# Kernel tuning notes

Hardware: AMD Instinct MI355X
Metric: run time of the kernel (lower is better)

## Reference

```python
import jax, jax.numpy as jnp
import numpy as np

D_MAIN = 512
D_BLOCK = 1024
N_NUM = 50
N_CAT = 20
N_FREQ = 16
D_EMB = 16
D_IN = N_NUM * D_EMB + N_CAT  # 820
EPS = 1e-5


def _ln(x, g, b):
    m = jnp.mean(x, -1, keepdims=True)
    v = jnp.mean((x - m) ** 2, -1, keepdims=True)
    return (x - m) * jax.lax.rsqrt(v + EPS) * g + b


def _encode(x_num, x_cat, freq, plr_w, plr_b, lin_w, lin_b,
            enc_w1, enc_b1, enc_w2, enc_b2, mix_g, mix_b, K_w, K_b):
    # PLR embeddings (lite): (B, F) -> (B, F, 2*n_freq) -> (B, F, d_emb) -> flatten
    p = 2.0 * jnp.pi * freq[None] * x_num[..., None]          # (B, F, n_freq)
    e = jnp.concatenate([jnp.cos(p), jnp.sin(p)], -1)          # (B, F, 2*n_freq)
    e = jax.nn.relu(e @ plr_w + plr_b)                         # (B, F, d_emb)
    x = jnp.concatenate([e.reshape(x_num.shape[0], -1), x_cat], 1)  # (B, d_in)
    x = x @ lin_w + lin_b                                      # (B, d_main)
    # encoder block 0 (no prenorm since i == 0); dropouts are 0 in eval
    x = x + (jax.nn.relu(x @ enc_w1 + enc_b1) @ enc_w2 + enc_b2)
    k = _ln(x, mix_g, mix_b) @ K_w + K_b                       # mixer normalization then K
    return x, k


def setup_inputs() -> dict:
    key = jax.random.key(0)
    ks = jax.random.split(key, 40)
    s = 0.02
    inp = {
        "x_num": jax.random.normal(ks[0], (512, N_NUM), jnp.float32),
        "x_cat": jax.random.uniform(ks[1], (512, N_CAT), jnp.float32),
        "candidate_x_num": jax.random.normal(ks[2], (50000, N_NUM), jnp.float32),
        "candidate_x_cat": jax.random.uniform(ks[3], (50000, N_CAT), jnp.float32),
        "candidate_y": jax.random.normal(ks[4], (50000,), jnp.float32),
        "context_size": 96,
        # PLR embedding params
        "freq": jax.random.normal(ks[5], (N_NUM, N_FREQ), jnp.float32) * 0.1,
        "plr_w": jax.random.normal(ks[6], (2 * N_FREQ, D_EMB), jnp.float32) * s,
        "plr_b": jnp.zeros((D_EMB,), jnp.float32),
        # input linear
        "lin_w": jax.random.normal(ks[7], (D_IN, D_MAIN), jnp.float32) * s,
        "lin_b": jnp.zeros((D_MAIN,), jnp.float32),
        # encoder block 0
        "enc_w1": jax.random.normal(ks[8], (D_MAIN, D_BLOCK), jnp.float32) * s,
        "enc_b1": jnp.zeros((D_BLOCK,), jnp.float32),
        "enc_w2": jax.random.normal(ks[9], (D_BLOCK, D_MAIN), jnp.float32) * s,
        "enc_b2": jnp.zeros((D_MAIN,), jnp.float32),
        # mixer normalization
        "mix_g": jnp.ones((D_MAIN,), jnp.float32),
        "mix_b": jnp.zeros((D_MAIN,), jnp.float32),
        # K projection
        "K_w": jax.random.normal(ks[10], (D_MAIN, D_MAIN), jnp.float32) * s,
        "K_b": jnp.zeros((D_MAIN,), jnp.float32),
        # label encoder Linear(1, d_main), uniform(-1/sqrt(2), 1/sqrt(2))
        "label_w": jax.random.uniform(ks[11], (D_MAIN,), jnp.float32, -0.7071, 0.7071),
        "label_b": jax.random.uniform(ks[12], (D_MAIN,), jnp.float32, -0.7071, 0.7071),
        # T transform
        "T_w1": jax.random.normal(ks[13], (D_MAIN, D_BLOCK), jnp.float32) * s,
        "T_b1": jnp.zeros((D_BLOCK,), jnp.float32),
        "T_w2": jax.random.normal(ks[14], (D_BLOCK, D_MAIN), jnp.float32) * s,
        # predictor block (prenorm)
        "pred_g": jnp.ones((D_MAIN,), jnp.float32),
        "pred_b": jnp.zeros((D_MAIN,), jnp.float32),
        "pred_w1": jax.random.normal(ks[15], (D_MAIN, D_BLOCK), jnp.float32) * s,
        "pred_b1": jnp.zeros((D_BLOCK,), jnp.float32),
        "pred_w2": jax.random.normal(ks[16], (D_BLOCK, D_MAIN), jnp.float32) * s,
        "pred_b2": jnp.zeros((D_MAIN,), jnp.float32),
        # head: LayerNorm -> ReLU -> Linear(d_main, 1)
        "head_g": jnp.ones((D_MAIN,), jnp.float32),
        "head_b": jnp.zeros((D_MAIN,), jnp.float32),
        "head_w": jax.random.normal(ks[17], (D_MAIN, 1), jnp.float32) * s,
        "head_bias": jnp.zeros((1,), jnp.float32),
    }
    return inp


def reference(x_num, x_cat, candidate_x_num, candidate_x_cat, candidate_y, context_size,
              freq, plr_w, plr_b, lin_w, lin_b, enc_w1, enc_b1, enc_w2, enc_b2,
              mix_g, mix_b, K_w, K_b, label_w, label_b, T_w1, T_b1, T_w2,
              pred_g, pred_b, pred_w1, pred_b1, pred_w2, pred_b2,
              head_g, head_b, head_w, head_bias):
    enc = lambda xn, xc: _encode(xn, xc, freq, plr_w, plr_b, lin_w, lin_b,
                                 enc_w1, enc_b1, enc_w2, enc_b2, mix_g, mix_b, K_w, K_b)
    # candidate keys cached under no_grad in the original
    cand_k = jax.lax.stop_gradient(enc(candidate_x_num, candidate_x_cat)[1])  # (N, D)
    x, k = enc(x_num, x_cat)                                                  # (B, D)
    # exact L2 kNN (= FAISS GpuIndexFlatL2), under no_grad
    kq = jax.lax.stop_gradient(k)
    d2 = (jnp.sum(kq * kq, -1, keepdims=True)
          - 2.0 * kq @ cand_k.T
          + jnp.sum(cand_k * cand_k, -1))                                     # (B, N)
    _, ctx_idx = jax.lax.top_k(-d2, context_size)                             # (B, C)
    ctx_k = cand_k[ctx_idx]                                                   # (B, C, D)
    # differentiable similarities (negative squared L2)
    sim = (-jnp.sum(k * k, -1, keepdims=True)
           + 2.0 * jnp.einsum('bd,bcd->bc', k, ctx_k)
           - jnp.sum(ctx_k * ctx_k, -1))                                      # (B, C)
    probs = jax.nn.softmax(sim, -1)                                           # (B, C)
    ctx_y = candidate_y[ctx_idx]                                              # (B, C)
    y_emb = ctx_y[..., None] * label_w + label_b                              # (B, C, D)
    diff = k[:, None, :] - ctx_k                                              # (B, C, D)
    values = y_emb + jax.nn.relu(diff @ T_w1 + T_b1) @ T_w2                   # (B, C, D)
    x = x + jnp.einsum('bc,bcd->bd', probs, values)
    # predictor block (prenorm)
    h = _ln(x, pred_g, pred_b)
    x = x + (jax.nn.relu(h @ pred_w1 + pred_b1) @ pred_w2 + pred_b2)
    # head
    return jax.nn.relu(_ln(x, head_g, head_b)) @ head_w + head_bias           # (B, 1)
```

## Files before the change

kernel.cpp:

```cpp
#include <hip/hip_runtime.h>

#define NCAND 50000
#define NB    512
#define DIN   820
#define KP_IN 832
#define DM    512
#define DBK   1024
#define NFEAT 50
#define NCAT  20
#define NFREQ 16
#define DEMB  16
#define CTX   96
#define NCMAX 9216
#define TOTMAX (NCMAX + CTX)

typedef __attribute__((ext_vector_type(8))) short short8;
typedef __attribute__((ext_vector_type(4))) float f32x4;

static __device__ __forceinline__ unsigned short f2bf(float f) {
    union { float f; unsigned int i; } u; u.f = f;
    unsigned int r = u.i + 0x7FFFu + ((u.i >> 16) & 1u);
    return (unsigned short)(r >> 16);
}
static __device__ __forceinline__ float bf2f(unsigned short s) {
    union { unsigned int i; float f; } u; u.i = ((unsigned int)s) << 16;
    return u.f;
}
static __device__ __forceinline__ unsigned int f2key(float f) {
    union { float f; unsigned int i; } u; u.f = f;
    return (u.i & 0x80000000u) ? ~u.i : (u.i | 0x80000000u);
}
static __device__ __forceinline__ float key2f(unsigned int k) {
    union { unsigned int i; float f; } u;
    u.i = (k & 0x80000000u) ? (k ^ 0x80000000u) : ~k;
    return u.f;
}

#define GLDS16(g, l) __builtin_amdgcn_global_load_lds( \
    (const __attribute__((address_space(1))) void*)(g), \
    (__attribute__((address_space(3))) void*)(l), 16, 0, 0)

#define BG_RELU  1
#define BG_SCORE 2

static __device__ __forceinline__ int swizzle_blk(int L, int nbx, int nby, int bigx,
                                                  int* bx, int* by)
{
    int nsm = bigx ? nby : nbx;
    int xcd = L & 7, slot = L >> 3;
    int big = xcd + 8 * (slot / nsm);
    int sml = slot % nsm;
    *bx = bigx ? big : sml;
    *by = bigx ? sml : big;
    return (*bx < nbx) && (*by < nby);
}

__global__ __launch_bounds__(256) void wprep_kernel(
    const float* __restrict__ W, int K, int N, int Kp,
    unsigned short* __restrict__ Wh, unsigned short* __restrict__ Wl)
{
    int idx = blockIdx.x * 256 + threadIdx.x;
    if (idx >= N * Kp) return;
    int n = idx / Kp, k = idx % Kp;
    float v = (k < K) ? W[(size_t)k * N + n] : 0.f;
    unsigned short h = f2bf(v);
    Wh[idx] = h;
    if (Wl) Wl[idx] = f2bf(v - bf2f(h));
}

__global__ __launch_bounds__(256) void plr_bf16_kernel(
    const float* __restrict__ xn_, const float* __restrict__ xc_, int nrows,
    const float* __restrict__ freq, const float* __restrict__ plr_w,
    const float* __restrict__ plr_b,
    unsigned short* __restrict__ oh, unsigned short* __restrict__ ol)
{
    __shared__ float sW[32 * 16];
    __shared__ float sB[16];
    __shared__ float sF[NFEAT * NFREQ];
    int tid = threadIdx.x;
    for (int i = tid; i < 512; i += 256) sW[i] = plr_w[i];
    if (tid < 16) sB[tid] = plr_b[tid];
    for (int i = tid; i < NFEAT * NFREQ; i += 256) sF[i] = freq[i];
    __syncthreads();
    int wave = tid >> 6, lane = tid & 63;
    int row = blockIdx.x * 4 + wave;
    if (row >= nrows) return;
    const float* xn = xn_ + (size_t)row * NFEAT;
    const float* xc = xc_ + (size_t)row * NCAT;
    unsigned short* ph = oh + (size_t)row * KP_IN;
    unsigned short* pl = ol + (size_t)row * KP_IN;
    if (lane < NFEAT) {
        float x = xn[lane];
        float cs[NFREQ], sn[NFREQ];
        #pragma unroll
        for (int j = 0; j < NFREQ; j++) {
            float p = 6.28318530717958647692f * sF[lane * NFREQ + j] * x;
            sn[j] = __sinf(p);
            cs[j] = __cosf(p);
        }
        #pragma unroll
        for (int d = 0; d < DEMB; d++) {
            float acc = sB[d];
            #pragma unroll
            for (int j = 0; j < NFREQ; j++)
                acc = fmaf(cs[j], sW[j * DEMB + d], fmaf(sn[j], sW[(NFREQ + j) * DEMB + d], acc));
            float v = fmaxf(acc, 0.f);
            unsigned short h = f2bf(v);
            ph[lane * DEMB + d] = h;
            pl[lane * DEMB + d] = f2bf(v - bf2f(h));
        }
    }
    if (lane < NCAT) {
        float v = xc[lane];
        unsigned short h = f2bf(v);
        ph[800 + lane] = h;
        pl[800 + lane] = f2bf(v - bf2f(h));
    }
    if (lane >= NCAT && lane < 32) {
        ph[800 + lane] = 0;
        pl[800 + lane] = 0;
    }
}

__global__ __launch_bounds__(512) void bgemm_kernel(
    const unsigned short* __restrict__ A, const unsigned short* __restrict__ Bt,
    int M, int N, int Kp, int nbx, int nby, int bigx,
    float* __restrict__ Cf, unsigned short* __restrict__ Cb,
    const float* __restrict__ bias, int flags)
{
    __shared__ unsigned short SH[2][2][128 * 32];
    int bxi, byi;
    if (!swizzle_blk(blockIdx.x, nbx, nby, bigx, &bxi, &byi)) return;
    int tid = threadIdx.x;
    int w = tid >> 6, lane = tid & 63;
    int m0 = byi * 128, n0 = bxi * 128;
    int wr = (w >> 1) * 32, wc = (w & 1) * 64;

    f32x4 acc[2][4];
    #pragma unroll
    for (int i = 0; i < 2; i++)
        #pragma unroll
        for (int j = 0; j < 4; j++) acc[i][j] = (f32x4){0.f, 0.f, 0.f, 0.f};

    int arr = w & 1;
    int qrt = (w >> 1) * 32;
    int scol = (((lane & 3) - ((lane >> 3) & 3)) & 3) * 8;
    const unsigned short* gsrc = arr ? Bt : A;
    int glim = arr ? (N - 1) : (M - 1);
    int gb   = arr ? n0 : m0;
    const unsigned short* gp0 = gsrc + (size_t)min(gb + qrt + (lane >> 2),      glim) * Kp + scol;
    const unsigned short* gp1 = gsrc + (size_t)min(gb + qrt + 16 + (lane >> 2), glim) * Kp + scol;
    int lo0 = qrt * 32, lo1 = (qrt + 16) * 32;

    int fr = lane & 15, q = lane >> 4;
    int pcs = ((q + (fr >> 1)) & 3) * 8;
    int niter = Kp >> 5;

    GLDS16(gp0, &SH[0][arr][lo0]);
    GLDS16(gp1, &SH[0][arr][lo1]);

    for (int it = 0; it < niter; it++) {
        __syncthreads();
        int bsel = it & 1;
        if (it + 1 < niter) {
            int k1 = (it + 1) << 5;
            GLDS16(gp0 + k1, &SH[bsel ^ 1][arr][lo0]);
            GLDS16(gp1 + k1, &SH[bsel ^ 1][arr][lo1]);
        }
        const unsigned short* As = SH[bsel][0];
        const unsigned short* Bs = SH[bsel][1];
        short8 a[2], b[4];
        #pragma unroll
        for (int i = 0; i < 2; i++)
            a[i] = *(const short8*)&As[(wr + i * 16 + fr) * 32 + pcs];
        #pragma unroll
        for (int j = 0; j < 4; j++)
            b[j] = *(const short8*)&Bs[(wc + j * 16 + fr) * 32 + pcs];
        #pragma unroll
        for (int i = 0; i < 2; i++)
            #pragma unroll
            for (int j = 0; j < 4; j++)
                acc[i][j] = __builtin_amdgcn_mfma_f32_16x16x32_bf16(a[i], b[j], acc[i][j], 0, 0, 0);
    }

    int col = lane & 15, rq = (lane >> 4) * 4;
    #pragma unroll
    for (int i = 0; i < 2; i++)
        #pragma unroll
        for (int j = 0; j < 4; j++) {
            int n_g = n0 + wc + j * 16 + col;
            #pragma unroll
            for (int r = 0; r < 4; r++) {
                int m_g = m0 + wr + i * 16 + rq + r;
                if (m_g < M && n_g < N) {
                    float v = acc[i][j][r];
                    if (bias) v += bias[n_g];
                    if (flags & BG_RELU) v = fmaxf(v, 0.f);
                    if (Cf) Cf[(size_t)m_g * N + n_g] = v;
                    if (Cb) Cb[(size_t)m_g * N + n_g] = f2bf(v);
                }
            }
        }
}

__global__ __launch_bounds__(512) void bgemm3_kernel(
    const unsigned short* __restrict__ Ah, const unsigned short* __restrict__ Al,
    const unsigned short* __restrict__ Bh, const unsigned short* __restrict__ Bl,
    int M, int N, int Kp, int nbx, int nby, int bigx,
    float* __restrict__ Cf, unsigned short* __restrict__ Cbh, unsigned short* __restrict__ Cbl,
    const float* __restrict__ bias, const float* __restrict__ resf,
    const float* __restrict__ cnorm, int flags)
{
    __shared__ unsigned short SH[2][4][128 * 32];
    int bxi, byi;
    if (!swizzle_blk(blockIdx.x, nbx, nby, bigx, &bxi, &byi)) return;
    int tid = threadIdx.x;
    int w = tid >> 6, lane = tid & 63;
    int m0 = byi * 128, n0 = bxi * 128;
    int wr = (w >> 1) * 32, wc = (w & 1) * 64;

    f32x4 acc[2][4];
    #pragma unroll
    for (int i = 0; i < 2; i++)
        #pragma unroll
        for (int j = 0; j < 4; j++) acc[i][j] = (f32x4){0.f, 0.f, 0.f, 0.f};

    int arr = w & 3;
    int half = (w >> 2) * 64;
    int scol = (((lane & 3) - ((lane >> 3) & 3)) & 3) * 8;
    const unsigned short* gsrc = (arr == 0) ? Ah : (arr == 1) ? Al : (arr == 2) ? Bh : Bl;
    int glim = (arr < 2) ? (M - 1) : (N - 1);
    int gb   = (arr < 2) ? m0 : n0;
    const unsigned short* gp[4];
    int lofs[4];
    #pragma unroll
    for (int t = 0; t < 4; t++) {
        int r = half + t * 16;
        gp[t] = gsrc + (size_t)min(gb + r + (lane >> 2), glim) * Kp + scol;
        lofs[t] = r * 32;
    }

    int fr = lane & 15, q = lane >> 4;
    int pcs = ((q + (fr >> 1)) & 3) * 8;
    int niter = Kp >> 5;

    #pragma unroll
    for (int t = 0; t < 4; t++) GLDS16(gp[t], &SH[0][arr][lofs[t]]);

    for (int it = 0; it < niter; it++) {
        __syncthreads();
        int bsel = it & 1;
        if (it + 1 < niter) {
            int k1 = (it + 1) << 5;
            #pragma unroll
            for (int t = 0; t < 4; t++) GLDS16(gp[t] + k1, &SH[bsel ^ 1][arr][lofs[t]]);
        }
        const unsigned short* Ash = SH[bsel][0];
        const unsigned short* Asl = SH[bsel][1];
        const unsigned short* Bsh = SH[bsel][2];
        const unsigned short* Bsl = SH[bsel][3];
        short8 a[2], b[4];
        #pragma unroll
        for (int i = 0; i < 2; i++)
            a[i] = *(const short8*)&Ash[(wr + i * 16 + fr) * 32 + pcs];
        #pragma unroll
        for (int j = 0; j < 4; j++)
            b[j] = *(const short8*)&Bsh[(wc + j * 16 + fr) * 32 + pcs];
        #pragma unroll
        for (int i = 0; i < 2; i++)
            #pragma unroll
            for (int j = 0; j < 4; j++)
                acc[i][j] = __builtin_amdgcn_mfma_f32_16x16x32_bf16(a[i], b[j], acc[i][j], 0, 0, 0);
        short8 al2[2];
        #pragma unroll
        for (int i = 0; i < 2; i++)
            al2[i] = *(const short8*)&Asl[(wr + i * 16 + fr) * 32 + pcs];
        #pragma unroll
        for (int i = 0; i < 2; i++)
            #pragma unroll
            for (int j = 0; j < 4; j++)
                acc[i][j] = __builtin_amdgcn_mfma_f32_16x16x32_bf16(al2[i], b[j], acc[i][j], 0, 0, 0);
        short8 bl2[4];
        #pragma unroll
        for (int j = 0; j < 4; j++)
            bl2[j] = *(const short8*)&Bsl[(wc + j * 16 + fr) * 32 + pcs];
        #pragma unroll
        for (int i = 0; i < 2; i++)
            #pragma unroll
            for (int j = 0; j < 4; j++)
                acc[i][j] = __builtin_amdgcn_mfma_f32_16x16x32_bf16(a[i], bl2[j], acc[i][j], 0, 0, 0);
    }

    int col = lane & 15, rq = (lane >> 4) * 4;
    #pragma unroll
    for (int i = 0; i < 2; i++)
        #pragma unroll
        for (int j = 0; j < 4; j++) {
            int n_g = n0 + wc + j * 16 + col;
            #pragma unroll
            for (int r = 0; r < 4; r++) {
                int m_g = m0 + wr + i * 16 + rq + r;
                if (m_g < M && n_g < N) {
                    float v = acc[i][j][r];
                    if (bias) v += bias[n_g];
                    if (resf) v += resf[(size_t)m_g * N + n_g];
                    if (flags & BG_RELU) v = fmaxf(v, 0.f);
                    if (flags & BG_SCORE) v = 2.f * v - cnorm[n_g];
                    if (Cf) Cf[(size_t)m_g * N + n_g] = v;
                    if (Cbh) {
                        unsigned short h = f2bf(v);
                        Cbh[(size_t)m_g * N + n_g] = h;
                        if (Cbl) Cbl[(size_t)m_g * N + n_g] = f2bf(v - bf2f(h));
                    }
                }
            }
        }
}

__global__ __launch_bounds__(256) void bgemm3s_kernel(
    const unsigned short* __restrict__ Ah, const unsigned short* __restrict__ Al,
    const unsigned short* __restrict__ Bh, const unsigned short* __restrict__ Bl,
    int M, int N, int Kp,
    float* __restrict__ Cf, unsigned short* __restrict__ Cbh, unsigned short* __restrict__ Cbl,
    const float* __restrict__ bias, const float* __restrict__ resf, int flags)
{
    __shared__ unsigned short Ash[64 * 32];
    __shared__ unsigned short Asl[64 * 32];
    __shared__ unsigned short Bsh[64 * 32];
    __shared__ unsigned short Bsl[64 * 32];
    int tid = threadIdx.x;
    int w = tid >> 6, lane = tid & 63;
    int m0 = blockIdx.y * 64, n0 = blockIdx.x * 64;
    int wr = (w >> 1) * 32, wc = (w & 1) * 32;
    int three = (Al != nullptr);

    f32x4 acc[2][2];
    #pragma unroll
    for (int i = 0; i < 2; i++)
        #pragma unroll
        for (int j = 0; j < 2; j++) acc[i][j] = (f32x4){0.f, 0.f, 0.f, 0.f};

    int srow = w * 16 + (lane >> 2);
    int scol = (((lane & 3) - ((lane >> 3) & 3)) & 3) * 8;
    size_t ra = (size_t)min(m0 + srow, M - 1) * Kp + scol;
    size_t rb = (size_t)min(n0 + srow, N - 1) * Kp + scol;
    unsigned short* lah = &Ash[(w * 16) * 32];
    unsigned short* lal = &Asl[(w * 16) * 32];
    unsigned short* lbh = &Bsh[(w * 16) * 32];
    unsigned short* lbl = &Bsl[(w * 16) * 32];

    int fr = lane & 15, q = lane >> 4;
    int pcs = ((q + (fr >> 1)) & 3) * 8;

    for (int k0 = 0; k0 < Kp; k0 += 32) {
        __syncthreads();
        GLDS16(Ah + ra + k0, lah);
        GLDS16(Bh + rb + k0, lbh);
        if (three) {
            GLDS16(Al + ra + k0, lal);
            GLDS16(Bl + rb + k0, lbl);
        }
        __syncthreads();
        short8 a[2], b[2];
        #pragma unroll
        for (int i = 0; i < 2; i++)
            a[i] = *(const short8*)&Ash[(wr + i * 16 + fr) * 32 + pcs];
        #pragma unroll
        for (int j = 0; j < 2; j++)
            b[j] = *(const short8*)&Bsh[(wc + j * 16 + fr) * 32 + pcs];
        #pragma unroll
        for (int i = 0; i < 2; i++)
            #pragma unroll
            for (int j = 0; j < 2; j++)
                acc[i][j] = __builtin_amdgcn_mfma_f32_16x16x32_bf16(a[i], b[j], acc[i][j], 0, 0, 0);
        if (three) {
            short8 al2[2], bl2[2];
            #pragma unroll
            for (int i = 0; i < 2; i++)
                al2[i] = *(const short8*)&Asl[(wr + i * 16 + fr) * 32 + pcs];
            #pragma unroll
            for (int j = 0; j < 2; j++)
                bl2[j] = *(const short8*)&Bsl[(wc + j * 16 + fr) * 32 + pcs];
            #pragma unroll
            for (int i = 0; i < 2; i++)
                #pragma unroll
                for (int j = 0; j < 2; j++) {
                    acc[i][j] = __builtin_amdgcn_mfma_f32_16x16x32_bf16(al2[i], b[j], acc[i][j], 0, 0, 0);
                    acc[i][j] = __builtin_amdgcn_mfma_f32_16x16x32_bf16(a[i], bl2[j], acc[i][j], 0, 0, 0);
                }
        }
    }

    int col = lane & 15, rq = (lane >> 4) * 4;
    #pragma unroll
    for (int i = 0; i < 2; i++)
        #pragma unroll
        for (int j = 0; j < 2; j++) {
            int n_g = n0 + wc + j * 16 + col;
            #pragma unroll
            for (int r = 0; r < 4; r++) {
                int m_g = m0 + wr + i * 16 + rq + r;
                if (m_g < M && n_g < N) {
                    float v = acc[i][j][r];
                    if (bias) v += bias[n_g];
                    if (resf) v += resf[(size_t)m_g * N + n_g];
                    if (flags & BG_RELU) v = fmaxf(v, 0.f);
                    if (Cf) Cf[(size_t)m_g * N + n_g] = v;
                    if (Cbh) {
                        unsigned short h = f2bf(v);
                        Cbh[(size_t)m_g * N + n_g] = h;
                        if (Cbl) Cbl[(size_t)m_g * N + n_g] = f2bf(v - bf2f(h));
                    }
                }
            }
        }
}

__global__ __launch_bounds__(256) void ln_split_kernel(const float* __restrict__ X,
    unsigned short* __restrict__ Yh, unsigned short* __restrict__ Yl,
    const float* __restrict__ g, const float* __restrict__ bt, int M)
{
    int wave = threadIdx.x >> 6, lane = threadIdx.x & 63;
    int row = blockIdx.x * 4 + wave;
    if (row >= M) return;
    const float* x = X + (size_t)row * DM;
    float4 v0 = ((const float4*)x)[lane * 2];
    float4 v1 = ((const float4*)x)[lane * 2 + 1];
    float s = v0.x + v0.y + v0.z + v0.w + v1.x + v1.y + v1.z + v1.w;
    #pragma unroll
    for (int off = 32; off; off >>= 1) s += __shfl_xor(s, off, 64);
    float m = s * (1.f / DM);
    float q = (v0.x - m) * (v0.x - m) + (v0.y - m) * (v0.y - m)
            + (v0.z - m) * (v0.z - m) + (v0.w - m) * (v0.w - m)
            + (v1.x - m) * (v1.x - m) + (v1.y - m) * (v1.y - m)
            + (v1.z - m) * (v1.z - m) + (v1.w - m) * (v1.w - m);
    #pragma unroll
    for (int off = 32; off; off >>= 1) q += __shfl_xor(q, off, 64);
    float rstd = 1.f / sqrtf(q * (1.f / DM) + 1e-5f);
    float vals[8] = {v0.x, v0.y, v0.z, v0.w, v1.x, v1.y, v1.z, v1.w};
    unsigned short* yh = Yh + (size_t)row * DM + lane * 8;
    unsigned short* yl = Yl + (size_t)row * DM + lane * 8;
    const float* gp = g + lane * 8;
    const float* bp = bt + lane * 8;
    #pragma unroll
    for (int i = 0; i < 8; i++) {
        float y = (vals[i] - m) * rstd * gp[i] + bp[i];
        unsigned short h = f2bf(y);
        yh[i] = h;
        yl[i] = f2bf(y - bf2f(h));
    }
}

__global__ __launch_bounds__(256) void cnorm_kernel(const float* __restrict__ Kc,
    float* __restrict__ cn, int N)
{
    int wave = threadIdx.x >> 6, lane = threadIdx.x & 63;
    int row = blockIdx.x * 4 + wave;
    if (row >= N) return;
    const float* x = Kc + (size_t)row * DM;
    float4 v0 = ((const float4*)x)[lane * 2];
    float4 v1 = ((const float4*)x)[lane * 2 + 1];
    float s = v0.x * v0.x + v0.y * v0.y + v0.z * v0.z + v0.w * v0.w
            + v1.x * v1.x + v1.y * v1.y + v1.z * v1.z + v1.w * v1.w;
    #pragma unroll
    for (int off = 32; off; off >>= 1) s += __shfl_xor(s, off, 64);
    if (lane == 0) cn[row] = s;
}

__global__ void ctx_init_kernel(int* __restrict__ idx, float* __restrict__ sc)
{
    int i = blockIdx.x * 256 + threadIdx.x;
    if (i < NB * CTX) { idx[i] = 0; sc[i] = -1e30f; }
}

#define CANDCAP 2048
__global__ __launch_bounds__(256) void topk_merge_kernel(
    const float* __restrict__ S, int m, int base,
    const int* __restrict__ pidx, const float* __restrict__ pscore,
    int* __restrict__ nidx, float* __restrict__ nscore)
{
    __shared__ __align__(16) unsigned int ks[TOTMAX];
    __shared__ unsigned int hist[4 * 256];
    __shared__ unsigned int sfx[256];
    __shared__ unsigned int s_prefix;
    __shared__ int s_above;
    __shared__ int prev_i[CTX];
    __shared__ int nsel, neq;
    __shared__ float sel_s[CTX];
    __shared__ int   sel_g[CTX];
    __shared__ int   cnd_g[CANDCAP];

    int b = blockIdx.x, tid = threadIdx.x;
    int lane = tid & 63, wv = tid >> 6;
    const float* Sb = S + (size_t)b * m;
    int tot = m + CTX;

    int m4 = m >> 2;
    const float4* S4 = (const float4*)Sb;
    for (int i = tid; i < m4; i += 256) {
        float4 v = S4[i];
        uint4 kk;
        kk.x = f2key(v.x); kk.y = f2key(v.y); kk.z = f2key(v.z); kk.w = f2key(v.w);
        ((uint4*)ks)[i] = kk;
    }
    for (int i = (m4 << 2) + tid; i < m; i += 256) ks[i] = f2key(Sb[i]);
    if (tid < CTX) {
        ks[m + tid] = f2key(pscore[b * CTX + tid]);
        prev_i[tid] = pidx[b * CTX + tid];
    }
    if (tid == 0) { s_prefix = 0u; s_above = 0; nsel = 0; neq = 0; }
    __syncthreads();

    unsigned int* myhist = &hist[wv * 256];

    for (int pass = 0; pass < 4; pass++) {
        int shift = 24 - pass * 8;
        for (int i = tid; i < 1024; i += 256) hist[i] = 0;
        __syncthreads();
        unsigned int pref = s_prefix;
        unsigned int msk = (pass == 0) ? 0u : (0xFFFFFFFFu << (32 - 8 * pass));
        for (int i0 = 0; i0 < tot; i0 += 256) {
            int i = i0 + tid;
            int pred = 0, digit = 0;
            if (i < tot) {
                unsigned int k = ks[i];
                pred = ((k & msk) == pref);
                digit = (int)((k >> shift) & 255u);
            }
            unsigned long long act = __ballot(pred);
            if (!act) continue;
            int lead = (int)__ffsll(act) - 1;
            int d0 = __shfl(digit, lead, 64);
            unsigned long long same = __ballot(pred && (digit == d0));
            if (same == act) {
                if (lane == lead) atomicAdd(&myhist[d0], (unsigned int)__popcll(act));
            } else {
                if (pred) atomicAdd(&myhist[digit], 1u);
            }
        }
        __syncthreads();
        unsigned int hb = hist[tid] + hist[256 + tid] + hist[512 + tid] + hist[768 + tid];
        __syncthreads();
        hist[tid] = hb;
        sfx[tid] = hb;
        __syncthreads();
        #pragma unroll
        for (int offd = 1; offd < 256; offd <<= 1) {
            unsigned int v = (tid + offd < 256) ? sfx[tid + offd] : 0u;
            __syncthreads();
            sfx[tid] += v;
            __syncthreads();
        }
        {
            int incl = s_above + (int)sfx[tid];
            int excl = incl - (int)hb;
            if (excl < CTX && incl >= CTX) {
                s_prefix = pref | ((unsigned int)tid << shift);
                s_above = excl;
            }
        }
        __syncthreads();
    }
    unsigned int thrK = s_prefix;
    int msel = CTX - s_above;
    float eqv = key2f(thrK);

    for (int i = tid; i < tot; i += 256) {
        unsigned int k = ks[i];
        if (k < thrK) continue;
        int g = (i < m) ? (base + i) : prev_i[i - m];
        if (k > thrK) {
            int p = atomicAdd(&nsel, 1);
            sel_s[p] = key2f(k); sel_g[p] = g;
        } else {
            int p = atomicAdd(&neq, 1);
            if (p < CANDCAP) cnd_g[p] = g;
        }
    }
    __syncthreads();
    int ne = neq;
    if (ne <= CANDCAP) {
        for (int i = tid; i < ne; i += 256) {
            int gi = cnd_g[i];
            int rank = 0;
            for (int j = 0; j < ne; j++) rank += (cnd_g[j] < gi);
            if (rank < msel) {
                int p = atomicAdd(&nsel, 1);
                sel_s[p] = eqv; sel_g[p] = gi;
            }
        }
    } else {
        for (int i = tid; i < tot; i += 256) {
            if (ks[i] != thrK) continue;
            int g = (i < m) ? (base + i) : prev_i[i - m];
            int rank = 0;
            for (int j = 0; j < tot; j++) {
                if (ks[j] == thrK) {
                    int gj = (j < m) ? (base + j) : prev_i[j - m];
                    rank += (gj < g);
                }
            }
            if (rank < msel) {
                int p = atomicAdd(&nsel, 1);
                sel_s[p] = eqv; sel_g[p] = g;
            }
        }
    }
    __syncthreads();
    if (tid < CTX) {
        nidx[b * CTX + tid] = sel_g[tid];
        nscore[b * CTX + tid] = sel_s[tid];
    }
}

__global__ __launch_bounds__(256) void agg_kernel(
    const int* __restrict__ ctx_idx, const float* __restrict__ ctx_score,
    const float* __restrict__ cand_y, const float* __restrict__ T1b,
    const unsigned short* __restrict__ T1c, const float* __restrict__ T_b1,
    const float* __restrict__ x_batch,
    const float* __restrict__ label_w, const float* __restrict__ label_b,
    unsigned short* __restrict__ s_h, unsigned short* __restrict__ s_l,
    float* __restrict__ u_out)
{
    __shared__ float p_s[CTX];
    __shared__ int   p_i[CTX];
    __shared__ float s_ybar;
    int b = blockIdx.x, tid = threadIdx.x;
    if (tid < CTX) { p_s[tid] = ctx_score[b * CTX + tid]; p_i[tid] = ctx_idx[b * CTX + tid]; }
    __syncthreads();
    if (tid == 0) {
        float mx = -1e30f;
        for (int c = 0; c < CTX; c++) mx = fmaxf(mx, p_s[c]);
        float sum = 0.f;
        for (int c = 0; c < CTX; c++) { float e = __expf(p_s[c] - mx); p_s[c] = e; sum += e; }
        float inv = 1.f / sum, yb = 0.f;
        for (int c = 0; c < CTX; c++) { p_s[c] *= inv; yb += p_s[c] * cand_y[p_i[c]]; }
        s_ybar = yb;
    }
    __syncthreads();
    int j = tid * 4;
    float4 kv = *(const float4*)(T1b + (size_t)b * DBK + j);
    float4 tb = *(const float4*)(T_b1 + j);
    float base0 = kv.x + tb.x, base1 = kv.y + tb.y, base2 = kv.z + tb.z, base3 = kv.w + tb.w;
    float a0 = 0.f, a1 = 0.f, a2 = 0.f, a3 = 0.f;
    for (int c = 0; c < CTX; c++) {
        float p = p_s[c];
        ushort4 cu = *(const ushort4*)(T1c + (size_t)p_i[c] * DBK + j);
        a0 = fmaf(p, fmaxf(base0 - bf2f(cu.x), 0.f), a0);
        a1 = fmaf(p, fmaxf(base1 - bf2f(cu.y), 0.f), a1);
        a2 = fmaf(p, fmaxf(base2 - bf2f(cu.z), 0.f), a2);
        a3 = fmaf(p, fmaxf(base3 - bf2f(cu.w), 0.f), a3);
    }
    {
        ushort4 oh, ol;
        oh.x = f2bf(a0); ol.x = f2bf(a0 - bf2f(oh.x));
        oh.y = f2bf(a1); ol.y = f2bf(a1 - bf2f(oh.y));
        oh.z = f2bf(a2); ol.z = f2bf(a2 - bf2f(oh.z));
        oh.w = f2bf(a3); ol.w = f2bf(a3 - bf2f(oh.w));
        *(ushort4*)(s_h + (size_t)b * DBK + j) = oh;
        *(ushort4*)(s_l + (size_t)b * DBK + j) = ol;
    }
    if (tid < 128) {
        int d = tid * 4;
        float4 xv = *(const float4*)(x_batch + (size_t)b * DM + d);
        float4 lw = *(const float4*)(label_w + d);
        float4 lb = *(const float4*)(label_b + d);
        float yb = s_ybar;
        *(float4*)(u_out + (size_t)b * DM + d) =
            make_float4(xv.x + yb * lw.x + lb.x, xv.y + yb * lw.y + lb.y,
                        xv.z + yb * lw.z + lb.z, xv.w + yb * lw.w + lb.w);
    }
}

__global__ __launch_bounds__(256) void head_kernel(
    const float* __restrict__ X, const float* __restrict__ g,
    const float* __restrict__ bt, const float* __restrict__ w,
    const float* __restrict__ hb, float* __restrict__ out, int M)
{
    int wave = threadIdx.x >> 6, lane = threadIdx.x & 63;
    int row = blockIdx.x * 4 + wave;
    if (row >= M) return;
    const float* x = X + (size_t)row * DM;
    float4 v0 = ((const float4*)x)[lane * 2];
    float4 v1 = ((const float4*)x)[lane * 2 + 1];
    float s = v0.x + v0.y + v0.z + v0.w + v1.x + v1.y + v1.z + v1.w;
    #pragma unroll
    for (int off = 32; off; off >>= 1) s += __shfl_xor(s, off, 64);
    float m = s * (1.f / DM);
    float q = (v0.x - m) * (v0.x - m) + (v0.y - m) * (v0.y - m)
            + (v0.z - m) * (v0.z - m) + (v0.w - m) * (v0.w - m)
            + (v1.x - m) * (v1.x - m) + (v1.y - m) * (v1.y - m)
            + (v1.z - m) * (v1.z - m) + (v1.w - m) * (v1.w - m);
    #pragma unroll
    for (int off = 32; off; off >>= 1) q += __shfl_xor(q, off, 64);
    float rstd = 1.f / sqrtf(q * (1.f / DM) + 1e-5f);
    float4 g0 = ((const float4*)g)[lane * 2], g1 = ((const float4*)g)[lane * 2 + 1];
    float4 b0 = ((const float4*)bt)[lane * 2], b1 = ((const float4*)bt)[lane * 2 + 1];
    float4 w0 = ((const float4*)w)[lane * 2], w1 = ((const float4*)w)[lane * 2 + 1];
    float t = 0.f;
    t += fmaxf((v0.x - m) * rstd * g0.x + b0.x, 0.f) * w0.x;
    t += fmaxf((v0.y - m) * rstd * g0.y + b0.y, 0.f) * w0.y;
    t += fmaxf((v0.z - m) * rstd * g0.z + b0.z, 0.f) * w0.z;
    t += fmaxf((v0.w - m) * rstd * g0.w + b0.w, 0.f) * w0.w;
    t += fmaxf((v1.x - m) * rstd * g1.x + b1.x, 0.f) * w1.x;
    t += fmaxf((v1.y - m) * rstd * g1.y + b1.y, 0.f) * w1.y;
    t += fmaxf((v1.z - m) * rstd * g1.z + b1.z, 0.f) * w1.z;
    t += fmaxf((v1.w - m) * rstd * g1.w + b1.w, 0.f) * w1.w;
    #pragma unroll
    for (int off = 32; off; off >>= 1) t += __shfl_xor(t, off, 64);
    if (lane == 0) out[row] = t + hb[0];
}

extern "C" void kernel_launch(void* const* d_in, const int* in_sizes, int n_in,
                              void* d_out, int out_size, void* d_ws, size_t ws_size,
                              hipStream_t stream) {
    (void)in_sizes; (void)n_in; (void)out_size;
    const float* x_num   = (const float*)d_in[0];
    const float* x_cat   = (const float*)d_in[1];
    const float* cxn     = (const float*)d_in[2];
    const float* cxc     = (const float*)d_in[3];
    const float* cand_y  = (const float*)d_in[4];
    const float* freq    = (const float*)d_in[6];
    const float* plr_w   = (const float*)d_in[7];
    const float* plr_b   = (const float*)d_in[8];
    const float* lin_w   = (const float*)d_in[9];
    const float* lin_b   = (const float*)d_in[10];
    const float* enc_w1  = (const float*)d_in[11];
    const float* enc_b1  = (const float*)d_in[12];
    const float* enc_w2  = (const float*)d_in[13];
    const float* enc_b2  = (const float*)d_in[14];
    const float* mix_g   = (const float*)d_in[15];
    const float* mix_b   = (const float*)d_in[16];
    const float* K_w     = (const float*)d_in[17];
    const float* K_b     = (const float*)d_in[18];
    const float* label_w = (const float*)d_in[19];
    const float* label_b = (const float*)d_in[20];
    const float* T_w1    = (const float*)d_in[21];
    const float* T_b1    = (const float*)d_in[22];
    const float* T_w2    = (const float*)d_in[23];
    const float* pred_g  = (const float*)d_in[24];
    const float* pred_b  = (const float*)d_in[25];
    const float* pred_w1 = (const float*)d_in[26];
    const float* pred_b1 = (const float*)d_in[27];
    const float* pred_w2 = (const float*)d_in[28];
    const float* pred_b2 = (const float*)d_in[29];
    const float* head_g  = (const float*)d_in[30];
    const float* head_b  = (const float*)d_in[31];
    const float* head_w  = (const float*)d_in[32];
    const float* head_bias = (const float*)d_in[33];
    float* out = (float*)d_out;

    char* ws = (char*)d_ws;
    size_t off = 0;
    auto alloc = [&](size_t n) { char* p = ws + off; off = (off + n + 255) & ~(size_t)255; return p; };

    typedef unsigned short u16;
    u16* lin_wt_h = (u16*)alloc((size_t)DM * KP_IN * 2);
    u16* lin_wt_l = (u16*)alloc((size_t)DM * KP_IN * 2);
    u16* e1t_h    = (u16*)alloc((size_t)DBK * DM * 2);
    u16* e1t_l    = (u16*)alloc((size_t)DBK * DM * 2);
    u16* e2t_h    = (u16*)alloc((size_t)DM * DBK * 2);
    u16* e2t_l    = (u16*)alloc((size_t)DM * DBK * 2);
    u16* K_wt_h   = (u16*)alloc((size_t)DM * DM * 2);
    u16* K_wt_l   = (u16*)alloc((size_t)DM * DM * 2);
    u16* T_w1t    = (u16*)alloc((size_t)DBK * DM * 2);
    u16* T_w2t_h  = (u16*)alloc((size_t)DM * DBK * 2);
    u16* T_w2t_l  = (u16*)alloc((size_t)DM * DBK * 2);
    u16* p1t_h    = (u16*)alloc((size_t)DBK * DM * 2);
    u16* p1t_l    = (u16*)alloc((size_t)DBK * DM * 2);
    u16* p2t_h    = (u16*)alloc((size_t)DM * DBK * 2);
    u16* p2t_l    = (u16*)alloc((size_t)DM * DBK * 2);
    u16*   T1c  = (u16*)alloc((size_t)NCAND * DBK * 2);
    float* T1b  = (float*)alloc((size_t)NB * DBK * 4);
    float* xB   = (float*)alloc((size_t)NB * DM * 4);
    u16*   kBh  = (u16*)alloc((size_t)NB * DM * 2);
    u16*   kBl  = (u16*)alloc((size_t)NB * DM * 2);
    u16* binh = (u16*)alloc((size_t)NB * KP_IN * 2);
    u16* binl = (u16*)alloc((size_t)NB * KP_IN * 2);
    u16* xBhh = (u16*)alloc((size_t)NB * DM * 2);
    u16* xBhl = (u16*)alloc((size_t)NB * DM * 2);
    u16* hBh  = (u16*)alloc((size_t)NB * DBK * 2);
    u16* hBl  = (u16*)alloc((size_t)NB * DBK * 2);
    u16* lnBh = (u16*)alloc((size_t)NB * DM * 2);
    u16* lnBl = (u16*)alloc((size_t)NB * DM * 2);
    int*   ctxAi = (int*)alloc((size_t)NB * CTX * 4);
    float* ctxAs = (float*)alloc((size_t)NB * CTX * 4);
    int*   ctxBi = (int*)alloc((size_t)NB * CTX * 4);
    float* ctxBs = (float*)alloc((size_t)NB * CTX * 4);
    u16*   sbufh = (u16*)alloc((size_t)NB * DBK * 2);
    u16*   sbufl = (u16*)alloc((size_t)NB * DBK * 2);
    float* ubuf  = (float*)alloc((size_t)NB * DM * 4);
    float* x2    = (float*)alloc((size_t)NB * DM * 4);
    u16*   h2h   = (u16*)alloc((size_t)NB * DM * 2);
    u16*   h2l   = (u16*)alloc((size_t)NB * DM * 2);
    u16*   hph   = (u16*)alloc((size_t)NB * DBK * 2);
    u16*   hpl   = (u16*)alloc((size_t)NB * DBK * 2);
    float* x3    = (float*)alloc((size_t)NB * DM * 4);

    size_t remain = (ws_size > off + 8192) ? (ws_size - off - 8192) : 0;
    const size_t perrow = 3328 + 2048 + 2048 + 4096 + 64;
    long ncl = (long)(remain / perrow);
    int NC = (int)(ncl > NCMAX ? NCMAX : ncl);
    NC &= ~127;
    if (NC < 256) NC = 256;
    char* arenaA = alloc((size_t)NC * 3328);
    char* arenaB = alloc((size_t)NC * 2048);
    char* arenaC = alloc((size_t)NC * 2048);
    char* arenaD = alloc((size_t)NC * 4096);
    u16* inCh = (u16*)arenaA;
    u16* inCl = inCh + (size_t)NC * KP_IN;
    float* kC  = (float*)arenaA;
    float* cnC = (float*)(arenaA + (size_t)NC * 2048);
    float* xC  = (float*)arenaB;
    float* scoresC = (float*)arenaB;
    u16* xCh  = (u16*)arenaC;
    u16* xCl  = xCh + (size_t)NC * DM;
    u16* lnCh = (u16*)arenaC;
    u16* lnCl = lnCh + (size_t)NC * DM;
    u16* hCh  = (u16*)arenaD;
    u16* hCl  = hCh + (size_t)NC * DBK;
    u16* kCh  = (u16*)arenaD;
    u16* kCl  = kCh + (size_t)NC * DM;

    auto bgemm = [&](const u16* A, const u16* Bt, int M, int N, int Kp,
                     float* Cf, u16* Cb, const float* bias, int flags) {
        int nbx = (N + 127) / 128, nby = (M + 127) / 128;
        int npad = (nby + 7) & ~7;
        bgemm_kernel<<<npad * nbx, 512, 0, stream>>>(A, Bt, M, N, Kp, nbx, nby, 0,
                                                     Cf, Cb, bias, flags);
    };
    auto bgemm3 = [&](const u16* Ah, const u16* Al, const u16* Bh, const u16* Bl,
                      int M, int N, int Kp, int bigx, float* Cf, u16* Cbh, u16* Cbl,
                      const float* bias, const float* resf, const float* cnorm, int flags) {
        int nbx = (N + 127) / 128, nby = (M + 127) / 128;
        int nbig = bigx ? nbx : nby, nsm = bigx ? nby : nbx;
        int npad = (nbig + 7) & ~7;
        bgemm3_kernel<<<npad * nsm, 512, 0, stream>>>(Ah, Al, Bh, Bl, M, N, Kp,
                                                      nbx, nby, bigx,
                                                      Cf, Cbh, Cbl, bias, resf, cnorm, flags);
    };
    auto bgemm3s = [&](const u16* Ah, const u16* Al, const u16* Bh, const u16* Bl,
                       int M, int N, int Kp, float* Cf, u16* Cbh, u16* Cbl,
                       const float* bias, const float* resf, int flags) {
        dim3 grid((N + 63) / 64, (M + 63) / 64);
        bgemm3s_kernel<<<grid, 256, 0, stream>>>(Ah, Al, Bh, Bl, M, N, Kp,
                                                 Cf, Cbh, Cbl, bias, resf, flags);
    };
    auto wprep = [&](const float* W, int K, int N, int Kp, u16* Wh, u16* Wl) {
        int n = N * Kp;
        wprep_kernel<<<(n + 255) / 256, 256, 0, stream>>>(W, K, N, Kp, Wh, Wl);
    };

    wprep(lin_w, DIN, DM, KP_IN, lin_wt_h, lin_wt_l);
    wprep(enc_w1, DM, DBK, DM, e1t_h, e1t_l);
    wprep(enc_w2, DBK, DM, DBK, e2t_h, e2t_l);
    wprep(K_w, DM, DM, DM, K_wt_h, K_wt_l);
    wprep(T_w1, DM, DBK, DM, T_w1t, nullptr);
    wprep(T_w2, DBK, DM, DBK, T_w2t_h, T_w2t_l);
    wprep(pred_w1, DM, DBK, DM, p1t_h, p1t_l);
    wprep(pred_w2, DBK, DM, DBK, p2t_h, p2t_l);

    plr_bf16_kernel<<<(NB + 3) / 4, 256, 0, stream>>>(x_num, x_cat, NB, freq, plr_w, plr_b, binh, binl);
    bgemm3s(binh, binl, lin_wt_h, lin_wt_l, NB, DM, KP_IN, xB, xBhh, xBhl, lin_b, nullptr, 0);
    bgemm3s(xBhh, xBhl, e1t_h, e1t_l, NB, DBK, DM, nullptr, hBh, hBl, enc_b1, nullptr, BG_RELU);
    bgemm3s(hBh, hBl, e2t_h, e2t_l, NB, DM, DBK, xB, nullptr, nullptr, enc_b2, xB, 0);
    ln_split_kernel<<<(NB + 3) / 4, 256, 0, stream>>>(xB, lnBh, lnBl, mix_g, mix_b, NB);
    bgemm3s(lnBh, lnBl, K_wt_h, K_wt_l, NB, DM, DM, nullptr, kBh, kBl, K_b, nullptr, 0);
    bgemm3s(kBh, nullptr, T_w1t, nullptr, NB, DBK, DM, T1b, nullptr, nullptr, nullptr, nullptr, 0);
    ctx_init_kernel<<<(NB * CTX + 255) / 256, 256, 0, stream>>>(ctxAi, ctxAs);

    const int* pI = ctxAi; const float* pS = ctxAs;
    int* nI = ctxBi; float* nS = ctxBs;
    int nch = (NCAND + NC - 1) / NC;
    for (int c = 0; c < nch; c++) {
        int s = c * NC;
        int m = NCAND - s; if (m > NC) m = NC;
        plr_bf16_kernel<<<(m + 3) / 4, 256, 0, stream>>>(cxn + (size_t)s * NFEAT,
                                                         cxc + (size_t)s * NCAT,
                                                         m, freq, plr_w, plr_b, inCh, inCl);
        bgemm3(inCh, inCl, lin_wt_h, lin_wt_l, m, DM, KP_IN, 0, xC, xCh, xCl, lin_b, nullptr, nullptr, 0);
        bgemm3(xCh, xCl, e1t_h, e1t_l, m, DBK, DM, 0, nullptr, hCh, hCl, enc_b1, nullptr, nullptr, BG_RELU);
        bgemm3(hCh, hCl, e2t_h, e2t_l, m, DM, DBK, 0, xC, nullptr, nullptr, enc_b2, xC, nullptr, 0);
        ln_split_kernel<<<(m + 3) / 4, 256, 0, stream>>>(xC, lnCh, lnCl, mix_g, mix_b, m);
        bgemm3(lnCh, lnCl, K_wt_h, K_wt_l, m, DM, DM, 0, kC, kCh, kCl, K_b, nullptr, nullptr, 0);
        cnorm_kernel<<<(m + 3) / 4, 256, 0, stream>>>(kC, cnC, m);
        bgemm(kCh, T_w1t, m, DBK, DM, nullptr, T1c + (size_t)s * DBK, nullptr, 0);
        bgemm3(kBh, kBl, kCh, kCl, NB, m, DM, 1, scoresC, nullptr, nullptr,
               nullptr, nullptr, cnC, BG_SCORE);
        topk_merge_kernel<<<NB, 256, 0, stream>>>(scoresC, m, s, pI, pS, nI, nS);
        { const int* t = pI; pI = nI; nI = (int*)t; }
        { const float* t = pS; pS = nS; nS = (float*)t; }
    }

    agg_kernel<<<NB, 256, 0, stream>>>(pI, pS, cand_y, T1b, T1c, T_b1,
                                       xB, label_w, label_b, sbufh, sbufl, ubuf);
    bgemm3s(sbufh, sbufl, T_w2t_h, T_w2t_l, NB, DM, DBK, x2, nullptr, nullptr,
            nullptr, ubuf, 0);
    ln_split_kernel<<<(NB + 3) / 4, 256, 0, stream>>>(x2, h2h, h2l, pred_g, pred_b, NB);
    bgemm3s(h2h, h2l, p1t_h, p1t_l, NB, DBK, DM, nullptr, hph, hpl, pred_b1, nullptr, BG_RELU);
    bgemm3s(hph, hpl, p2t_h, p2t_l, NB, DM, DBK, x3, nullptr, nullptr, pred_b2, x2, 0);
    head_kernel<<<(NB + 3) / 4, 256, 0, stream>>>(x3, head_g, head_b, head_w, head_bias, out, NB);
}
```

Before: 2.030 ms.

## Drop fp32 candidate intermediates, keep split-bf16 residuals, enlarge candidate chunks

The candidate encoder chain no longer writes fp32 copies of x and k. The residual add in bgemm3 now reads the hi/lo bf16 pair instead of an fp32 buffer, and layernorm and the candidate-norm kernel rebuild fp32 from those pairs. Removing one workspace arena frees memory, so the chunk cap is raised and the candidate loop runs fewer, larger iterations with fewer launches and top-k merges. The risks are small precision differences from the split-bf16 residual and the in-place layernorm, and a larger top-k shared-memory buffer, which may lower occupancy of the merge kernel.

```diff
diff --git a/kernel.cpp b/kernel.cpp
--- a/kernel.cpp
+++ b/kernel.cpp
@@ -11,7 +11,7 @@
 #define NFREQ 16
 #define DEMB  16
 #define CTX   96
-#define NCMAX 9216
+#define NCMAX 15872
 #define TOTMAX (NCMAX + CTX)
 
 typedef __attribute__((ext_vector_type(8))) short short8;
@@ -208,7 +208,8 @@
     const unsigned short* __restrict__ Bh, const unsigned short* __restrict__ Bl,
     int M, int N, int Kp, int nbx, int nby, int bigx,
     float* __restrict__ Cf, unsigned short* __restrict__ Cbh, unsigned short* __restrict__ Cbl,
-    const float* __restrict__ bias, const float* __restrict__ resf,
+    const float* __restrict__ bias,
+    const unsigned short* __restrict__ resh, const unsigned short* __restrict__ resl,
     const float* __restrict__ cnorm, int flags)
 {
     __shared__ unsigned short SH[2][4][128 * 32];
@@ -301,16 +302,17 @@
             for (int r = 0; r < 4; r++) {
                 int m_g = m0 + wr + i * 16 + rq + r;
                 if (m_g < M && n_g < N) {
+                    size_t idx = (size_t)m_g * N + n_g;
                     float v = acc[i][j][r];
                     if (bias) v += bias[n_g];
-                    if (resf) v += resf[(size_t)m_g * N + n_g];
+                    if (resh) v += bf2f(resh[idx]) + bf2f(resl[idx]);
                     if (flags & BG_RELU) v = fmaxf(v, 0.f);
                     if (flags & BG_SCORE) v = 2.f * v - cnorm[n_g];
-                    if (Cf) Cf[(size_t)m_g * N + n_g] = v;
+                    if (Cf) Cf[idx] = v;
                     if (Cbh) {
                         unsigned short h = f2bf(v);
-                        Cbh[(size_t)m_g * N + n_g] = h;
-                        if (Cbl) Cbl[(size_t)m_g * N + n_g] = f2bf(v - bf2f(h));
+                        Cbh[idx] = h;
+                        if (Cbl) Cbl[idx] = f2bf(v - bf2f(h));
                     }
                 }
             }
@@ -451,17 +453,70 @@
     }
 }
 
-__global__ __launch_bounds__(256) void cnorm_kernel(const float* __restrict__ Kc,
+__global__ __launch_bounds__(256) void ln_split2_kernel(
+    const unsigned short* __restrict__ Xh, const unsigned short* __restrict__ Xl,
+    unsigned short* __restrict__ Yh, unsigned short* __restrict__ Yl,
+    const float* __restrict__ g, const float* __restrict__ bt, int M)
+{
+    int wave = threadIdx.x >> 6, lane = threadIdx.x & 63;
+    int row = blockIdx.x * 4 + wave;
+    if (row >= M) return;
+    const ushort4* xh = (const ushort4*)(Xh + (size_t)row * DM) + lane * 2;
+    const ushort4* xl = (const ushort4*)(Xl + (size_t)row * DM) + lane * 2;
+    ushort4 h0 = xh[0], h1 = xh[1];
+    ushort4 l0 = xl[0], l1 = xl[1];
+    float vals[8] = {
+        bf2f(h0.x) + bf2f(l0.x), bf2f(h0.y) + bf2f(l0.y),
+        bf2f(h0.z) + bf2f(l0.z), bf2f(h0.w) + bf2f(l0.w),
+        bf2f(h1.x) + bf2f(l1.x), bf2f(h1.y) + bf2f(l1.y),
+        bf2f(h1.z) + bf2f(l1.z), bf2f(h1.w) + bf2f(l1.w)
+    };
+    float s = 0.f;
+    #pragma unroll
+    for (int i = 0; i < 8; i++) s += vals[i];
+    #pragma unroll
+    for (int off = 32; off; off >>= 1) s += __shfl_xor(s, off, 64);
+    float m = s * (1.f / DM);
+    float q = 0.f;
+    #pragma unroll
+    for (int i = 0; i < 8; i++) q += (vals[i] - m) * (vals[i] - m);
+    #pragma unroll
+    for (int off = 32; off; off >>= 1) q += __shfl_xor(q, off, 64);
+    float rstd = 1.f / sqrtf(q * (1.f / DM) + 1e-5f);
+    unsigned short* yh = Yh + (size_t)row * DM + lane * 8;
+    unsigned short* yl = Yl + (size_t)row * DM + lane * 8;
+    const float* gp = g + lane * 8;
+    const float* bp = bt + lane * 8;
+    #pragma unroll
+    for (int i = 0; i < 8; i++) {
+        float y = (vals[i] - m) * rstd * gp[i] + bp[i];
+        unsigned short h = f2bf(y);
+        yh[i] = h;
+        yl[i] = f2bf(y - bf2f(h));
+    }
+}
+
+__global__ __launch_bounds__(256) void cnorm2_kernel(
+    const unsigned short* __restrict__ Kh, const unsigned short* __restrict__ Kl,
     float* __restrict__ cn, int N)
 {
     int wave = threadIdx.x >> 6, lane = threadIdx.x & 63;
     int row = blockIdx.x * 4 + wave;
     if (row >= N) return;
-    const float* x = Kc + (size_t)row * DM;
-    float4 v0 = ((const float4*)x)[lane * 2];
-    float4 v1 = ((const float4*)x)[lane * 2 + 1];
-    float s = v0.x * v0.x + v0.y * v0.y + v0.z * v0.z + v0.w * v0.w
-            + v1.x * v1.x + v1.y * v1.y + v1.z * v1.z + v1.w * v1.w;
+    const ushort4* xh = (const ushort4*)(Kh + (size_t)row * DM) + lane * 2;
+    const ushort4* xl = (const ushort4*)(Kl + (size_t)row * DM) + lane * 2;
+    ushort4 h0 = xh[0], h1 = xh[1];
+    ushort4 l0 = xl[0], l1 = xl[1];
+    float s = 0.f;
+    float v;
+    v = bf2f(h0.x) + bf2f(l0.x); s += v * v;
+    v = bf2f(h0.y) + bf2f(l0.y); s += v * v;
+    v = bf2f(h0.z) + bf2f(l0.z); s += v * v;
+    v = bf2f(h0.w) + bf2f(l0.w); s += v * v;
+    v = bf2f(h1.x) + bf2f(l1.x); s += v * v;
+    v = bf2f(h1.y) + bf2f(l1.y); s += v * v;
+    v = bf2f(h1.z) + bf2f(l1.z); s += v * v;
+    v = bf2f(h1.w) + bf2f(l1.w); s += v * v;
     #pragma unroll
     for (int off = 32; off; off >>= 1) s += __shfl_xor(s, off, 64);
     if (lane == 0) cn[row] = s;
@@ -798,25 +853,20 @@
     float* x3    = (float*)alloc((size_t)NB * DM * 4);
 
     size_t remain = (ws_size > off + 8192) ? (ws_size - off - 8192) : 0;
-    const size_t perrow = 3328 + 2048 + 2048 + 4096 + 64;
+    const size_t perrow = 3328 + 2048 + 4096 + 64;
     long ncl = (long)(remain / perrow);
     int NC = (int)(ncl > NCMAX ? NCMAX : ncl);
     NC &= ~127;
     if (NC < 256) NC = 256;
     char* arenaA = alloc((size_t)NC * 3328);
-    char* arenaB = alloc((size_t)NC * 2048);
     char* arenaC = alloc((size_t)NC * 2048);
     char* arenaD = alloc((size_t)NC * 4096);
     u16* inCh = (u16*)arenaA;
     u16* inCl = inCh + (size_t)NC * KP_IN;
-    float* kC  = (float*)arenaA;
+    float* scoresC = (float*)arenaA;
     float* cnC = (float*)(arenaA + (size_t)NC * 2048);
-    float* xC  = (float*)arenaB;
-    float* scoresC = (float*)arenaB;
     u16* xCh  = (u16*)arenaC;
     u16* xCl  = xCh + (size_t)NC * DM;
-    u16* lnCh = (u16*)arenaC;
-    u16* lnCl = lnCh + (size_t)NC * DM;
     u16* hCh  = (u16*)arenaD;
     u16* hCl  = hCh + (size_t)NC * DBK;
     u16* kCh  = (u16*)arenaD;
@@ -831,13 +881,15 @@
     };
     auto bgemm3 = [&](const u16* Ah, const u16* Al, const u16* Bh, const u16* Bl,
                       int M, int N, int Kp, int bigx, float* Cf, u16* Cbh, u16* Cbl,
-                      const float* bias, const float* resf, const float* cnorm, int flags) {
+                      const float* bias, const u16* resh, const u16* resl,
+                      const float* cnorm, int flags) {
         int nbx = (N + 127) / 128, nby = (M + 127) / 128;
         int nbig = bigx ? nbx : nby, nsm = bigx ? nby : nbx;
         int npad = (nbig + 7) & ~7;
         bgemm3_kernel<<<npad * nsm, 512, 0, stream>>>(Ah, Al, Bh, Bl, M, N, Kp,
                                                       nbx, nby, bigx,
-                                                      Cf, Cbh, Cbl, bias, resf, cnorm, flags);
+                                                      Cf, Cbh, Cbl, bias, resh, resl,
+                                                      cnorm, flags);
     };
     auto bgemm3s = [&](const u16* Ah, const u16* Al, const u16* Bh, const u16* Bl,
                        int M, int N, int Kp, float* Cf, u16* Cbh, u16* Cbl,
@@ -878,15 +930,19 @@
         plr_bf16_kernel<<<(m + 3) / 4, 256, 0, stream>>>(cxn + (size_t)s * NFEAT,
                                                          cxc + (size_t)s * NCAT,
                                                          m, freq, plr_w, plr_b, inCh, inCl);
-        bgemm3(inCh, inCl, lin_wt_h, lin_wt_l, m, DM, KP_IN, 0, xC, xCh, xCl, lin_b, nullptr, nullptr, 0);
-        bgemm3(xCh, xCl, e1t_h, e1t_l, m, DBK, DM, 0, nullptr, hCh, hCl, enc_b1, nullptr, nullptr, BG_RELU);
-        bgemm3(hCh, hCl, e2t_h, e2t_l, m, DM, DBK, 0, xC, nullptr, nullptr, enc_b2, xC, nullptr, 0);
-        ln_split_kernel<<<(m + 3) / 4, 256, 0, stream>>>(xC, lnCh, lnCl, mix_g, mix_b, m);
-        bgemm3(lnCh, lnCl, K_wt_h, K_wt_l, m, DM, DM, 0, kC, kCh, kCl, K_b, nullptr, nullptr, 0);
-        cnorm_kernel<<<(m + 3) / 4, 256, 0, stream>>>(kC, cnC, m);
+        bgemm3(inCh, inCl, lin_wt_h, lin_wt_l, m, DM, KP_IN, 0,
+               nullptr, xCh, xCl, lin_b, nullptr, nullptr, nullptr, 0);
+        bgemm3(xCh, xCl, e1t_h, e1t_l, m, DBK, DM, 0,
+               nullptr, hCh, hCl, enc_b1, nullptr, nullptr, nullptr, BG_RELU);
+        bgemm3(hCh, hCl, e2t_h, e2t_l, m, DM, DBK, 0,
+               nullptr, xCh, xCl, enc_b2, xCh, xCl, nullptr, 0);
+        ln_split2_kernel<<<(m + 3) / 4, 256, 0, stream>>>(xCh, xCl, xCh, xCl, mix_g, mix_b, m);
+        bgemm3(xCh, xCl, K_wt_h, K_wt_l, m, DM, DM, 0,
+               nullptr, kCh, kCl, K_b, nullptr, nullptr, nullptr, 0);
+        cnorm2_kernel<<<(m + 3) / 4, 256, 0, stream>>>(kCh, kCl, cnC, m);
         bgemm(kCh, T_w1t, m, DBK, DM, nullptr, T1c + (size_t)s * DBK, nullptr, 0);
         bgemm3(kBh, kBl, kCh, kCl, NB, m, DM, 1, scoresC, nullptr, nullptr,
-               nullptr, nullptr, cnC, BG_SCORE);
+               nullptr, nullptr, nullptr, cnC, BG_SCORE);
         topk_merge_kernel<<<NB, 256, 0, stream>>>(scoresC, m, s, pI, pS, nI, nS);
         { const int* t = pI; pI = nI; nI = (int*)t; }
         { const float* t = pS; pS = nS; nS = (float*)t; }
```

Measured after the change: 1.716 ms. 1.18x faster.
